# Optimization experiments

Hardware: AMD Instinct MI355X
Metric: run time of the kernel (lower is better)

## Reference

```python
import jax, jax.numpy as jnp
import numpy as np

B, L, D, V = 2, 1024, 128, 5

def setup_inputs() -> dict:
    key = jax.random.key(0)
    k1, k2, k3, k4 = jax.random.split(key, 4)
    x = jax.random.randint(k1, (B, L), 0, V)
    emb_table = jax.random.normal(k2, (V, D), dtype=jnp.float32)
    # torch Linear(2D -> D): weight [D, 2D], bias [D]
    W = jax.random.normal(k3, (D, 2 * D), dtype=jnp.float32) * (1.0 / np.sqrt(2 * D))
    b = jax.random.normal(k4, (D,), dtype=jnp.float32) * 0.01
    return {"x": x, "emb_table": emb_table, "W": W, "b": b}

def reference(x, emb_table, W, b):
    # s: [B, L, D] embedding lookup
    s = emb_table[x]
    # Linear on concat(m_i, m_j) == split weight: W1 acts on row-broadcast half,
    # W2 on column-broadcast half. Avoids materializing [B,L,L,2D].
    D_ = W.shape[0]
    W1, W2 = W[:, :D_], W[:, D_:]
    p1 = jnp.einsum('bld,ed->ble', s, W1)  # [B, L, D]
    p2 = jnp.einsum('bld,ed->ble', s, W2)  # [B, L, D]
    # m[b,i,j,:] = p1[b,i] + p2[b,j] + b ; then permute to [B, D, L, L]
    m = p1[:, :, None, :] + p2[:, None, :, :] + b
    m = jnp.transpose(m, (0, 3, 1, 2))
    return (s, m)
```

## Files before the change

kernel.cpp:

```cpp
#include <hip/hip_runtime.h>

#define Bq 2
#define Lq 1024
#define Dq 128
#define Vq 5

typedef __attribute__((ext_vector_type(4))) float float4v;

#define WS_FLAG_OFF 1280

__global__ void k_flag(const int* __restrict__ x32, int* __restrict__ flag) {
    __shared__ int red[256];
    const int t = threadIdx.x;
    int acc = 0;
    for (int k = t; k < 1024; k += 256)
        acc |= x32[2 * k + 1];
    red[t] = acc;
    __syncthreads();
    for (int s = 128; s > 0; s >>= 1) {
        if (t < s) red[t] |= red[t + s];
        __syncthreads();
    }
    if (t == 0) flag[0] = red[0];
}

__device__ __forceinline__ int x_at(const int* __restrict__ x32, int f, int idx) {
    return x32[f ? idx : 2 * idx];
}

__global__ void k_prep(const int* __restrict__ x32,
                       const float* __restrict__ emb,
                       const float* __restrict__ W,
                       const float* __restrict__ bias,
                       float* __restrict__ ws,
                       float* __restrict__ s_out) {
    const int bid = blockIdx.x;
    const int t   = threadIdx.x;
    if (bid < Vq) {
        const int v     = bid;
        const int which = t >> 7;
        const int e     = t & 127;
        float acc = which ? 0.0f : bias[e];
        const float* wrow = W + e * (2 * Dq) + which * Dq;
        const float* erow = emb + v * Dq;
        #pragma unroll 8
        for (int d = 0; d < Dq; ++d)
            acc += erow[d] * wrow[d];
        ws[which * (Vq * Dq) + v * Dq + e] = acc;
    } else {
        const int f    = ((const int*)ws)[WS_FLAG_OFF];
        const int sb   = bid - Vq;
        const int pair = t >> 4;
        const int dgrp = t & 15;
        const int bl   = sb * 16 + pair;
        const int v    = x_at(x32, f, bl);
        const float* src = emb + v * Dq + dgrp * 8;
        float*       dst = s_out + (size_t)bl * Dq + dgrp * 8;
        float4v a = *reinterpret_cast<const float4v*>(src);
        float4v b = *reinterpret_cast<const float4v*>(src + 4);
        *reinterpret_cast<float4v*>(dst)     = a;
        *reinterpret_cast<float4v*>(dst + 4) = b;
    }
}

__device__ __forceinline__ float sel5(const float p[5], int v) {
    float p_ = p[4];
    p_ = (v == 3) ? p[3] : p_;
    p_ = (v == 2) ? p[2] : p_;
    p_ = (v == 1) ? p[1] : p_;
    p_ = (v == 0) ? p[0] : p_;
    return p_;
}

__global__ void __launch_bounds__(256) k_m(const int* __restrict__ x32,
                                           const float* __restrict__ ws,
                                           float* __restrict__ m_out) {
    const int n  = blockIdx.x;
    const int t  = threadIdx.x;
    const int f  = ((const int*)ws)[WS_FLAG_OFF];
    const int l1 = n & 1023;
    const int hi = n >> 10;

    const int v1a = x_at(x32, f, l1);
    const int v1b = x_at(x32, f, Lq + l1);
    int va[4], vb[4];
    #pragma unroll
    for (int j = 0; j < 4; ++j) {
        va[j] = x_at(x32, f, 4 * t + j);
        vb[j] = x_at(x32, f, Lq + 4 * t + j);
    }

    const float* __restrict__ P1 = ws;
    const float* __restrict__ P2 = ws + Vq * Dq;

    #pragma unroll
    for (int half = 0; half < 2; ++half) {
        const int tok1 = half ? v1b : v1a;
        int tj[4];
        #pragma unroll
        for (int j = 0; j < 4; ++j) tj[j] = half ? vb[j] : va[j];

        #pragma unroll 4
        for (int i2 = 0; i2 < 64; ++i2) {
            const int i = half * 64 + i2;
            const int e = 2 * i2 + hi;
            float p1c[5], p2c[5];
            #pragma unroll
            for (int v = 0; v < 5; ++v) {
                p1c[v] = P1[v * Dq + e];
                p2c[v] = P2[v * Dq + e];
            }
            const float c1 = sel5(p1c, tok1);
            float4v o;
            #pragma unroll
            for (int j = 0; j < 4; ++j)
                o[j] = c1 + sel5(p2c, tj[j]);
            const size_t g = (size_t)i * 2048 + n;
            *reinterpret_cast<float4v*>(m_out + g * Lq + 4 * t) = o;
        }
    }
}

extern "C" void kernel_launch(void* const* d_in, const int* in_sizes, int n_in,
                              void* d_out, int out_size, void* d_ws, size_t ws_size,
                              hipStream_t stream) {
    const int*   x32  = (const int*)d_in[0];
    const float* emb  = (const float*)d_in[1];
    const float* W    = (const float*)d_in[2];
    const float* bias = (const float*)d_in[3];
    float* out   = (float*)d_out;
    float* ws    = (float*)d_ws;
    float* s_out = out;
    float* m_out = out + (size_t)Bq * Lq * Dq;

    k_flag<<<1, 256, 0, stream>>>(x32, ((int*)ws) + WS_FLAG_OFF);
    k_prep<<<Vq + (Bq * Lq / 16), 256, 0, stream>>>(x32, emb, W, bias, ws, s_out);
    k_m<<<Bq * Dq * (Lq / 128), 256, 0, stream>>>(x32, ws, m_out);
}
```

Measured before the change: 1.170 ms.

## Precompute per-row p1 terms and restructure output kernel by (batch, channel, row-chunk)

Adds a kernel that writes the p1 contribution for every (batch, channel, position) into workspace, so the main kernel no longer performs a 5-way select per output row. The output kernel now maps each block to one (batch, channel) and a 128-row chunk. Each thread computes its four column p2 values once, then streams contiguous rows using preloaded c1 values. This changes the write order to contiguous rows within one output plane, at the cost of an extra kernel launch and 1 MB of workspace traffic.

```diff
diff --git a/kernel.cpp b/kernel.cpp
--- a/kernel.cpp
+++ b/kernel.cpp
@@ -6,8 +6,10 @@
 #define Vq 5
 
 typedef __attribute__((ext_vector_type(4))) float float4v;
+typedef __attribute__((ext_vector_type(4))) int   int4v;
 
 #define WS_FLAG_OFF 1280
+#define WS_C1_OFF   2048
 
 __global__ void k_flag(const int* __restrict__ x32, int* __restrict__ flag) {
     __shared__ int red[256];
@@ -26,6 +28,15 @@
 
 __device__ __forceinline__ int x_at(const int* __restrict__ x32, int f, int idx) {
     return x32[f ? idx : 2 * idx];
+}
+
+__device__ __forceinline__ float sel5(const float p[5], int v) {
+    float p_ = p[4];
+    p_ = (v == 3) ? p[3] : p_;
+    p_ = (v == 2) ? p[2] : p_;
+    p_ = (v == 1) ? p[1] : p_;
+    p_ = (v == 0) ? p[0] : p_;
+    return p_;
 }
 
 __global__ void k_prep(const int* __restrict__ x32,
@@ -63,60 +74,72 @@
     }
 }
 
-__device__ __forceinline__ float sel5(const float p[5], int v) {
-    float p_ = p[4];
-    p_ = (v == 3) ? p[3] : p_;
-    p_ = (v == 2) ? p[2] : p_;
-    p_ = (v == 1) ? p[1] : p_;
-    p_ = (v == 0) ? p[0] : p_;
-    return p_;
+__global__ void k_c1(const int* __restrict__ x32,
+                     float* __restrict__ ws) {
+    const int bc = blockIdx.x;
+    const int e  = bc & 127;
+    const int b  = bc >> 7;
+    const int t  = threadIdx.x;
+    const int f  = ((const int*)ws)[WS_FLAG_OFF];
+    float p1c[5];
+    #pragma unroll
+    for (int v = 0; v < 5; ++v) p1c[v] = ws[v * Dq + e];
+    int vv[4];
+    if (f) {
+        int4v xv = *reinterpret_cast<const int4v*>(x32 + b * Lq + 4 * t);
+        vv[0] = xv[0]; vv[1] = xv[1]; vv[2] = xv[2]; vv[3] = xv[3];
+    } else {
+        #pragma unroll
+        for (int j = 0; j < 4; ++j) vv[j] = x_at(x32, 0, b * Lq + 4 * t + j);
+    }
+    float4v o;
+    #pragma unroll
+    for (int j = 0; j < 4; ++j) o[j] = sel5(p1c, vv[j]);
+    *reinterpret_cast<float4v*>(ws + WS_C1_OFF + (size_t)bc * Lq + 4 * t) = o;
 }
 
 __global__ void __launch_bounds__(256) k_m(const int* __restrict__ x32,
                                            const float* __restrict__ ws,
                                            float* __restrict__ m_out) {
-    const int n  = blockIdx.x;
-    const int t  = threadIdx.x;
-    const int f  = ((const int*)ws)[WS_FLAG_OFF];
-    const int l1 = n & 1023;
-    const int hi = n >> 10;
+    constexpr int CH = Lq / 128;
+    const int bid   = blockIdx.x;
+    const int chunk = bid % CH;
+    const int tmp   = bid / CH;
+    const int e     = tmp % Dq;
+    const int b     = tmp / Dq;
+    const int t     = threadIdx.x;
+    const int f     = ((const int*)ws)[WS_FLAG_OFF];
 
-    const int v1a = x_at(x32, f, l1);
-    const int v1b = x_at(x32, f, Lq + l1);
-    int va[4], vb[4];
+    float p2c[5];
     #pragma unroll
-    for (int j = 0; j < 4; ++j) {
-        va[j] = x_at(x32, f, 4 * t + j);
-        vb[j] = x_at(x32, f, Lq + 4 * t + j);
+    for (int v = 0; v < 5; ++v) p2c[v] = ws[Vq * Dq + v * Dq + e];
+    int vv[4];
+    if (f) {
+        int4v xv = *reinterpret_cast<const int4v*>(x32 + b * Lq + 4 * t);
+        vv[0] = xv[0]; vv[1] = xv[1]; vv[2] = xv[2]; vv[3] = xv[3];
+    } else {
+        #pragma unroll
+        for (int j = 0; j < 4; ++j) vv[j] = x_at(x32, 0, b * Lq + 4 * t + j);
     }
+    float c2[4];
+    #pragma unroll
+    for (int j = 0; j < 4; ++j) c2[j] = sel5(p2c, vv[j]);
 
-    const float* __restrict__ P1 = ws;
-    const float* __restrict__ P2 = ws + Vq * Dq;
+    const size_t row0 = (size_t)(b * Dq + e) * Lq + chunk * 128;
+    const float* __restrict__ c1T = ws + WS_C1_OFF + row0;
+    float* out_base = m_out + row0 * Lq + 4 * t;
 
-    #pragma unroll
-    for (int half = 0; half < 2; ++half) {
-        const int tok1 = half ? v1b : v1a;
-        int tj[4];
+    for (int c32 = 0; c32 < 4; ++c32) {
+        float c1v[32];
         #pragma unroll
-        for (int j = 0; j < 4; ++j) tj[j] = half ? vb[j] : va[j];
-
-        #pragma unroll 4
-        for (int i2 = 0; i2 < 64; ++i2) {
-            const int i = half * 64 + i2;
-            const int e = 2 * i2 + hi;
-            float p1c[5], p2c[5];
-            #pragma unroll
-            for (int v = 0; v < 5; ++v) {
-                p1c[v] = P1[v * Dq + e];
-                p2c[v] = P2[v * Dq + e];
-            }
-            const float c1 = sel5(p1c, tok1);
+        for (int k = 0; k < 32; ++k)
+            c1v[k] = c1T[c32 * 32 + k];
+        #pragma unroll
+        for (int k = 0; k < 32; ++k) {
             float4v o;
             #pragma unroll
-            for (int j = 0; j < 4; ++j)
-                o[j] = c1 + sel5(p2c, tj[j]);
-            const size_t g = (size_t)i * 2048 + n;
-            *reinterpret_cast<float4v*>(m_out + g * Lq + 4 * t) = o;
+            for (int j = 0; j < 4; ++j) o[j] = c1v[k] + c2[j];
+            *reinterpret_cast<float4v*>(out_base + (size_t)(c32 * 32 + k) * Lq) = o;
         }
     }
 }
@@ -135,5 +158,6 @@
 
     k_flag<<<1, 256, 0, stream>>>(x32, ((int*)ws) + WS_FLAG_OFF);
     k_prep<<<Vq + (Bq * Lq / 16), 256, 0, stream>>>(x32, emb, W, bias, ws, s_out);
+    k_c1<<<Bq * Dq, 256, 0, stream>>>(x32, ws);
     k_m<<<Bq * Dq * (Lq / 128), 256, 0, stream>>>(x32, ws, m_out);
 }
```

Measured after the change: 1.086 ms. -7.2%, faster.
